# Kernel optimization log

Hardware: AMD Instinct MI355X
Metric: run time of the kernel (lower is better)

The kernel has to match this reference:

```python
import jax, jax.numpy as jnp
import numpy as np

N, L, S, D, H = 4, 8192, 8192, 256, 8
HD = D // H
EPS_ATTN = 1e-6
EPS_LN = 1e-5


def _layer_norm(x, g, b):
    mu = jnp.mean(x, axis=-1, keepdims=True)
    var = jnp.mean((x - mu) ** 2, axis=-1, keepdims=True)
    return (x - mu) / jnp.sqrt(var + EPS_LN) * g + b


def setup_inputs() -> dict:
    key = jax.random.key(0)
    ks = jax.random.split(key, 12)
    sc = 1.0 / np.sqrt(D)
    sc2 = 1.0 / np.sqrt(2 * D)
    return {
        "x": jax.random.normal(ks[0], (N, L, D), jnp.float32),
        "source": jax.random.normal(ks[1], (N, S, D), jnp.float32),
        "x_mask": jnp.ones((N, L), jnp.float32),
        "source_mask": jnp.ones((N, S), jnp.float32),
        "Wq": jax.random.normal(ks[2], (D, D), jnp.float32) * sc,
        "Wk": jax.random.normal(ks[3], (D, D), jnp.float32) * sc,
        "Wv": jax.random.normal(ks[4], (D, D), jnp.float32) * sc,
        "Wm": jax.random.normal(ks[5], (D, D), jnp.float32) * sc,
        "W1": jax.random.normal(ks[6], (2 * D, 2 * D), jnp.float32) * sc2,
        "W2": jax.random.normal(ks[7], (D, 2 * D), jnp.float32) * sc2,
        "g1": jnp.ones((D,), jnp.float32),
        "b1": jnp.zeros((D,), jnp.float32),
        "g2": jnp.ones((D,), jnp.float32),
        "b2": jnp.zeros((D,), jnp.float32),
    }


def reference(x, source, x_mask, source_mask, Wq, Wk, Wv, Wm, W1, W2, g1, b1, g2, b2):
    n = x.shape[0]
    # QKV projections (Linear without bias: y = x @ W.T), split into heads
    q = (x @ Wq.T).reshape(n, -1, H, HD)         # [N, L, H, HD]
    k = (source @ Wk.T).reshape(n, -1, H, HD)    # [N, S, H, HD]
    v = (source @ Wv.T).reshape(n, -1, H, HD)    # [N, S, H, HD]

    # kernelized linear attention: phi(x) = elu(x) + 1
    Q = jax.nn.elu(q) + 1.0
    K = jax.nn.elu(k) + 1.0
    Q = Q * x_mask[:, :, None, None]
    K = K * source_mask[:, :, None, None]
    v = v * source_mask[:, :, None, None]

    s_len = v.shape[1]
    v = v / s_len
    KV = jnp.einsum('nshd,nshv->nhdv', K, v)                       # [N, H, HD, HD]
    Z = 1.0 / (jnp.einsum('nlhd,nhd->nlh', Q, K.sum(axis=1)) + EPS_ATTN)
    msg = jnp.einsum('nlhd,nhdv,nlh->nlhv', Q, KV, Z) * s_len      # [N, L, H, HD]

    # merge heads + LN
    msg = msg.reshape(n, -1, H * HD) @ Wm.T
    msg = _layer_norm(msg, g1, b1)

    # concat-MLP + LN + residual
    h = jnp.concatenate([x, msg], axis=2) @ W1.T
    h = jax.nn.relu(h) @ W2.T
    h = _layer_norm(h, g2, b2)
    return x + h
```

## Files before the change

kernel.cpp:

```cpp
#include <hip/hip_runtime.h>

using short8 = __attribute__((ext_vector_type(8))) short;
using f32x4  = __attribute__((ext_vector_type(4))) float;

__device__ __forceinline__ float bf2f(unsigned short u) {
  union { unsigned int i; float f; } c; c.i = ((unsigned int)u) << 16; return c.f;
}
__device__ __forceinline__ unsigned short f2bf(float x) {
  union { float f; unsigned int i; } c; c.f = x;
  unsigned int r = c.i + 0x7fffu + ((c.i >> 16) & 1u);
  return (unsigned short)(r >> 16);
}

__global__ void cast2_kernel(const float* __restrict__ a, const float* __restrict__ b,
                             unsigned short* __restrict__ oa, unsigned short* __restrict__ ob,
                             int n4) {
  int stride = gridDim.x * blockDim.x;
  for (int i = blockIdx.x * blockDim.x + threadIdx.x; i < 2 * n4; i += stride) {
    const float4* s; ushort4* d; int j;
    if (i < n4) { s = (const float4*)a; d = (ushort4*)oa; j = i; }
    else        { s = (const float4*)b; d = (ushort4*)ob; j = i - n4; }
    float4 v = s[j];
    ushort4 o; o.x = f2bf(v.x); o.y = f2bf(v.y); o.z = f2bf(v.z); o.w = f2bf(v.w);
    d[j] = o;
  }
}

__global__ void castw_kernel(const float* __restrict__ wq, const float* __restrict__ wk,
                             const float* __restrict__ wv, const float* __restrict__ wm,
                             const float* __restrict__ w1, const float* __restrict__ w2,
                             unsigned short* __restrict__ dst) {
  int i = blockIdx.x * blockDim.x + threadIdx.x;
  if (i >= 655360) return;
  const float* s; int off;
  if      (i < 65536)  { s = wq; off = i; }
  else if (i < 131072) { s = wk; off = i - 65536; }
  else if (i < 196608) { s = wv; off = i - 131072; }
  else if (i < 262144) { s = wm; off = i - 196608; }
  else if (i < 524288) { s = w1; off = i - 262144; }
  else                 { s = w2; off = i - 524288; }
  dst[i] = f2bf(s[off]);
}

enum { EPI_F32 = 0, EPI_ELU1_MASK = 1, EPI_KV = 2, EPI_RELU_BF16 = 3 };

template<int EPI, bool SPLITA>
__global__ __launch_bounds__(256)
void gemm_nt(const unsigned short* __restrict__ A, const unsigned short* __restrict__ A2,
             const unsigned short* __restrict__ B,
             void* __restrict__ C0, void* __restrict__ C1, const float* __restrict__ aux,
             int M, int O, int K, float scale) {
  __shared__ unsigned short As[128 * 64];
  __shared__ unsigned short Bs[128 * 64];
  const int t  = threadIdx.x;
  const int w  = t >> 6, l = t & 63;
  const int wr = w >> 1, wc = w & 1;
  const int lr = l & 15, kg = l >> 4;
  const int brow = blockIdx.x * 128, bcol = blockIdx.y * 128;
  const int rsub = l >> 3;
  const int swz  = 8 * ((l & 7) ^ rsub);

  f32x4 acc[4][4];
  f32x4 zero = {0.f, 0.f, 0.f, 0.f};
  #pragma unroll
  for (int m = 0; m < 4; m++)
    #pragma unroll
    for (int n = 0; n < 4; n++) acc[m][n] = zero;

  for (int k0 = 0; k0 < K; k0 += 64) {
    #pragma unroll
    for (int i = 0; i < 4; i++) {
      int c = w * 4 + i;
      int row = c * 8 + rsub;
      const unsigned short* ga;
      if (SPLITA) {
        const unsigned short* base = (k0 < 256) ? A : A2;
        ga = base + (size_t)(brow + row) * 256 + (k0 & 255) + swz;
      } else {
        ga = A + (size_t)(brow + row) * K + k0 + swz;
      }
      const unsigned short* gb = B + (size_t)(bcol + row) * K + k0 + swz;
      __builtin_amdgcn_global_load_lds((__attribute__((address_space(1))) unsigned int*)ga,
          (__attribute__((address_space(3))) unsigned int*)(As + c * 512), 16, 0, 0);
      __builtin_amdgcn_global_load_lds((__attribute__((address_space(1))) unsigned int*)gb,
          (__attribute__((address_space(3))) unsigned int*)(Bs + c * 512), 16, 0, 0);
    }
    __syncthreads();
    #pragma unroll
    for (int kk = 0; kk < 2; kk++) {
      short8 af[4], bfr[4];
      #pragma unroll
      for (int m = 0; m < 4; m++) {
        int r = wr * 64 + m * 16 + lr;
        int cb = kk * 64 + kg * 16;
        af[m] = *(const short8*)((const char*)As + r * 128 + (cb ^ ((r & 7) << 4)));
      }
      #pragma unroll
      for (int n = 0; n < 4; n++) {
        int r = wc * 64 + n * 16 + lr;
        int cb = kk * 64 + kg * 16;
        bfr[n] = *(const short8*)((const char*)Bs + r * 128 + (cb ^ ((r & 7) << 4)));
      }
      #pragma unroll
      for (int m = 0; m < 4; m++)
        #pragma unroll
        for (int n = 0; n < 4; n++)
          acc[m][n] = __builtin_amdgcn_mfma_f32_16x16x32_bf16(af[m], bfr[n], acc[m][n], 0, 0, 0);
    }
    __syncthreads();
  }

  #pragma unroll
  for (int m = 0; m < 4; m++) {
    #pragma unroll
    for (int n = 0; n < 4; n++) {
      int col = bcol + wc * 64 + n * 16 + lr;
      #pragma unroll
      for (int j = 0; j < 4; j++) {
        int row = brow + wr * 64 + m * 16 + kg * 4 + j;
        float v = acc[m][n][j];
        if (EPI == EPI_F32) {
          ((float*)C0)[(size_t)row * O + col] = v;
        } else if (EPI == EPI_ELU1_MASK) {
          float e = v > 0.f ? v + 1.f : __expf(v);
          ((unsigned short*)C0)[(size_t)row * O + col] = f2bf(e * aux[row]);
        } else if (EPI == EPI_KV) {
          int colm = col & 255;
          if (col < 256) {
            float e = v > 0.f ? v + 1.f : __expf(v);
            ((unsigned short*)C0)[(size_t)row * 256 + colm] = f2bf(e * aux[row]);
          } else {
            ((unsigned short*)C1)[(size_t)row * 256 + colm] = f2bf(v * aux[row] * scale);
          }
        } else {
          ((unsigned short*)C0)[(size_t)row * O + col] = f2bf(v > 0.f ? v : 0.f);
        }
      }
    }
  }
}

__global__ __launch_bounds__(1024)
void kv_partial(const unsigned short* __restrict__ Kb, const unsigned short* __restrict__ Vb,
                float* __restrict__ part_kv, float* __restrict__ part_ks) {
  __shared__ float Ks[16][256];
  __shared__ float Vs[16][256];
  const int t   = threadIdx.x;
  const int blk = blockIdx.x;
  const int n   = blk >> 6;
  const int s0  = (blk & 63) * 128;
  const int h   = t >> 7, g = (t >> 5) & 3, dv = t & 31;
  const int r16 = t >> 6, c4 = (t & 63) * 4;
  const int cbase = h * 32;
  f32x4 acc0 = {0.f, 0.f, 0.f, 0.f}, acc1 = {0.f, 0.f, 0.f, 0.f};
  float ks = 0.f;

  for (int tile = 0; tile < 8; ++tile) {
    int s = s0 + tile * 16;
    size_t gbase = ((size_t)(n * 8192 + s + r16)) * 256 + c4;
    ushort4 kk = *(const ushort4*)&Kb[gbase];
    ushort4 vv = *(const ushort4*)&Vb[gbase];
    __syncthreads();
    float4 kf; kf.x = bf2f(kk.x); kf.y = bf2f(kk.y); kf.z = bf2f(kk.z); kf.w = bf2f(kk.w);
    float4 vf; vf.x = bf2f(vv.x); vf.y = bf2f(vv.y); vf.z = bf2f(vv.z); vf.w = bf2f(vv.w);
    *(float4*)&Ks[r16][c4] = kf;
    *(float4*)&Vs[r16][c4] = vf;
    __syncthreads();
    if (t < 256) {
      #pragma unroll
      for (int r = 0; r < 16; ++r) ks += Ks[r][t];
    }
    #pragma unroll
    for (int si = 0; si < 16; ++si) {
      f32x4 k0 = *(const f32x4*)&Ks[si][cbase + g * 8];
      f32x4 k1 = *(const f32x4*)&Ks[si][cbase + g * 8 + 4];
      float vx = Vs[si][cbase + dv];
      acc0 += k0 * vx;
      acc1 += k1 * vx;
    }
  }
  float* dst = &part_kv[(size_t)blk * 8192 + h * 1024 + dv * 32 + g * 8];
  *(float4*)(dst + 0) = *(float4*)&acc0;
  *(float4*)(dst + 4) = *(float4*)&acc1;
  if (t < 256) part_ks[blk * 256 + t] = ks;
}

__global__ __launch_bounds__(1024)
void kv_finalize(const float* __restrict__ part_kv, const float* __restrict__ part_ks,
                 float* __restrict__ KVt, float* __restrict__ Ksum) {
  const int b = blockIdx.x, t = threadIdx.x;
  if (b < 32) {
    int n = b >> 3;
    int e = (b & 7) * 1024 + t;
    const float* p = part_kv + (size_t)n * 64 * 8192 + e;
    float s = 0.f;
    #pragma unroll 8
    for (int c = 0; c < 64; ++c) s += p[(size_t)c * 8192];
    KVt[(size_t)n * 8192 + e] = s;
  } else {
    int n = b - 32;
    if (t < 256) {
      const float* p = part_ks + n * 64 * 256 + t;
      float s = 0.f;
      #pragma unroll 8
      for (int c = 0; c < 64; ++c) s += p[c * 256];
      Ksum[n * 256 + t] = s;
    }
  }
}

__global__ __launch_bounds__(256)
void msg_apply(const unsigned short* __restrict__ Qb, const float* __restrict__ KVt,
               const float* __restrict__ Ksum, unsigned short* __restrict__ Mb) {
  __shared__ float KVs[8192];
  __shared__ float Kss[256];
  const int t = threadIdx.x;
  const int row0 = blockIdx.x * 32;
  const int n = blockIdx.x >> 8;
  const int r = t >> 3, h = t & 7;
  for (int i = t; i < 8192; i += 256) {
    int j = i ^ (((i >> 10) & 7) << 2);
    KVs[j] = KVt[(size_t)n * 8192 + i];
  }
  Kss[t] = Ksum[n * 256 + t];
  __syncthreads();

  const unsigned short* qp = &Qb[(size_t)(row0 + r) * 256 + h * 32];
  float q[32];
  #pragma unroll
  for (int i = 0; i < 4; ++i) {
    short8 v = *(const short8*)(qp + i * 8);
    #pragma unroll
    for (int j = 0; j < 8; ++j) q[i * 8 + j] = bf2f((unsigned short)v[j]);
  }
  float zden = 0.f;
  #pragma unroll
  for (int sl = 0; sl < 8; ++sl) {
    f32x4 kv = *(const f32x4*)&Kss[h * 32 + sl * 4];
    zden += q[sl*4+0]*kv[0] + q[sl*4+1]*kv[1] + q[sl*4+2]*kv[2] + q[sl*4+3]*kv[3];
  }
  float z = 8192.f / (zden + 1e-6f);
  const int kvbase = h * 1024;
  short8 ov[4];
  #pragma unroll
  for (int dv = 0; dv < 32; ++dv) {
    float o = 0.f;
    #pragma unroll
    for (int sl = 0; sl < 8; ++sl) {
      f32x4 kv = *(const f32x4*)&KVs[kvbase + dv * 32 + ((sl ^ h) << 2)];
      o += q[sl*4+0]*kv[0] + q[sl*4+1]*kv[1] + q[sl*4+2]*kv[2] + q[sl*4+3]*kv[3];
    }
    ov[dv >> 3][dv & 7] = (short)f2bf(o * z);
  }
  unsigned short* op = (unsigned short*)&Mb[(size_t)(row0 + r) * 256 + h * 32];
  #pragma unroll
  for (int i = 0; i < 4; ++i) *(short8*)(op + i * 8) = ov[i];
}

__device__ __forceinline__ float block_sum(float v, float* red) {
  #pragma unroll
  for (int o = 32; o; o >>= 1) v += __shfl_down(v, o, 64);
  __syncthreads();
  if ((threadIdx.x & 63) == 0) red[threadIdx.x >> 6] = v;
  __syncthreads();
  return red[0] + red[1] + red[2] + red[3];
}

__global__ __launch_bounds__(256)
void ln1_msg(const float* __restrict__ msgf, const float* __restrict__ g,
             const float* __restrict__ b, unsigned short* __restrict__ msgb) {
  __shared__ float red[4];
  int row = blockIdx.x, t = threadIdx.x;
  float v = msgf[(size_t)row * 256 + t];
  float mu  = block_sum(v, red) * (1.f / 256.f);
  float dvv = v - mu;
  float var = block_sum(dvv * dvv, red) * (1.f / 256.f);
  float y = dvv * rsqrtf(var + 1e-5f) * g[t] + b[t];
  msgb[(size_t)row * 256 + t] = f2bf(y);
}

__global__ __launch_bounds__(256)
void ln2_res(const float* __restrict__ hbuf, const float* __restrict__ x,
             const float* __restrict__ g, const float* __restrict__ b,
             float* __restrict__ out) {
  __shared__ float red[4];
  int row = blockIdx.x, t = threadIdx.x;
  float v = hbuf[(size_t)row * 256 + t];
  float mu  = block_sum(v, red) * (1.f / 256.f);
  float dvv = v - mu;
  float var = block_sum(dvv * dvv, red) * (1.f / 256.f);
  float y = dvv * rsqrtf(var + 1e-5f) * g[t] + b[t];
  out[(size_t)row * 256 + t] = x[(size_t)row * 256 + t] + y;
}

extern "C" void kernel_launch(void* const* d_in, const int* in_sizes, int n_in,
                              void* d_out, int out_size, void* d_ws, size_t ws_size,
                              hipStream_t stream) {
  const float* x   = (const float*)d_in[0];
  const float* src = (const float*)d_in[1];
  const float* xm  = (const float*)d_in[2];
  const float* sm  = (const float*)d_in[3];
  const float* Wq  = (const float*)d_in[4];
  const float* Wk  = (const float*)d_in[5];
  const float* Wv  = (const float*)d_in[6];
  const float* Wm  = (const float*)d_in[7];
  const float* W1  = (const float*)d_in[8];
  const float* W2  = (const float*)d_in[9];
  const float* g1  = (const float*)d_in[10];
  const float* b1  = (const float*)d_in[11];
  const float* g2  = (const float*)d_in[12];
  const float* b2  = (const float*)d_in[13];
  float* out = (float*)d_out;
  char*  ws  = (char*)d_ws;

  unsigned short* xb   = (unsigned short*)(ws);
  unsigned short* sb   = (unsigned short*)(ws + 16777216);
  unsigned short* Qb   = (unsigned short*)(ws + 33554432);
  unsigned short* Mb   = (unsigned short*)(ws + 50331648);
  unsigned short* Kb   = (unsigned short*)(ws + 67108864);
  unsigned short* Vb   = (unsigned short*)(ws + 83886080);
  float*          pkv  = (float*)(ws + 16777216);
  float*          pks  = (float*)(ws + 16777216 + 8388608);
  float*          msgf = (float*)(ws + 67108864);
  unsigned short* msgb = (unsigned short*)(ws + 50331648);
  unsigned short* h1b  = (unsigned short*)(ws + 67108864);
  float*          h2f  = (float*)(ws);
  float*          KV   = (float*)(ws + 100663296);
  float*          Ksm  = (float*)(ws + 100663296 + 131072);
  unsigned short* Wb   = (unsigned short*)(ws + 100663296 + 135168);
  unsigned short* Wqb = Wb;
  unsigned short* Wkb = Wb + 65536;
  unsigned short* Wmb = Wb + 196608;
  unsigned short* W1b = Wb + 262144;
  unsigned short* W2b = Wb + 524288;

  cast2_kernel<<<2048, 256, 0, stream>>>(x, src, xb, sb, 2097152);
  castw_kernel<<<2560, 256, 0, stream>>>(Wq, Wk, Wv, Wm, W1, W2, Wb);

  gemm_nt<EPI_ELU1_MASK, false><<<dim3(256, 2), 256, 0, stream>>>(
      xb, nullptr, Wqb, (void*)Qb, nullptr, xm, 32768, 256, 256, 0.f);
  gemm_nt<EPI_KV, false><<<dim3(256, 4), 256, 0, stream>>>(
      sb, nullptr, Wkb, (void*)Kb, (void*)Vb, sm, 32768, 512, 256, 1.f / 8192.f);

  kv_partial<<<256, 1024, 0, stream>>>(Kb, Vb, pkv, pks);
  kv_finalize<<<36, 1024, 0, stream>>>(pkv, pks, KV, Ksm);
  msg_apply<<<1024, 256, 0, stream>>>(Qb, KV, Ksm, Mb);

  gemm_nt<EPI_F32, false><<<dim3(256, 2), 256, 0, stream>>>(
      Mb, nullptr, Wmb, (void*)msgf, nullptr, nullptr, 32768, 256, 256, 0.f);
  ln1_msg<<<32768, 256, 0, stream>>>(msgf, g1, b1, msgb);

  gemm_nt<EPI_RELU_BF16, true><<<dim3(256, 4), 256, 0, stream>>>(
      xb, msgb, W1b, (void*)h1b, nullptr, nullptr, 32768, 512, 512, 0.f);
  gemm_nt<EPI_F32, false><<<dim3(256, 2), 256, 0, stream>>>(
      h1b, nullptr, W2b, (void*)h2f, nullptr, nullptr, 32768, 256, 512, 0.f);
  ln2_res<<<32768, 256, 0, stream>>>(h2f, x, g2, b2, out);
}
```

Before: 321.9 us.

## Fuse LayerNorm into full-row GEMM epilogues and merge cast kernels

Adds a gemm_ln kernel in which each 512-thread block owns 128 full 256-wide output rows. It computes LayerNorm statistics from the accumulators through shuffles and shared memory, then writes the normalized bf16 message, or the residual-added fp32 output, directly. This removes the fp32 intermediate round trips and the two separate per-row LN kernels. The two cast kernels are merged into one launch with vectorized weight casts. The trade-offs are fewer blocks per GEMM (256 blocks), a larger shared-memory footprint, and a one-pass variance formula (E[x²]-mu²) that is less numerically robust.

```diff
diff --git a/kernel.cpp b/kernel.cpp
--- a/kernel.cpp
+++ b/kernel.cpp
@@ -12,37 +12,41 @@
   return (unsigned short)(r >> 16);
 }
 
-__global__ void cast2_kernel(const float* __restrict__ a, const float* __restrict__ b,
-                             unsigned short* __restrict__ oa, unsigned short* __restrict__ ob,
-                             int n4) {
+__global__ void cast_all(const float* __restrict__ x, const float* __restrict__ src,
+                         const float* __restrict__ wq, const float* __restrict__ wk,
+                         const float* __restrict__ wv, const float* __restrict__ wm,
+                         const float* __restrict__ w1, const float* __restrict__ w2,
+                         unsigned short* __restrict__ xb, unsigned short* __restrict__ sb,
+                         unsigned short* __restrict__ Wb) {
+  const int NV = 2097152;
   int stride = gridDim.x * blockDim.x;
-  for (int i = blockIdx.x * blockDim.x + threadIdx.x; i < 2 * n4; i += stride) {
+  for (int i = blockIdx.x * blockDim.x + threadIdx.x; i < 2 * NV + 163840; i += stride) {
     const float4* s; ushort4* d; int j;
-    if (i < n4) { s = (const float4*)a; d = (ushort4*)oa; j = i; }
-    else        { s = (const float4*)b; d = (ushort4*)ob; j = i - n4; }
+    if (i < NV)            { s = (const float4*)x;   d = (ushort4*)xb; j = i; }
+    else if (i < 2 * NV)   { s = (const float4*)src; d = (ushort4*)sb; j = i - NV; }
+    else {
+      j = i - 2 * NV;
+      d = (ushort4*)Wb;
+      const float* w;
+      int off;
+      if      (j < 16384)  { w = wq; off = j; }
+      else if (j < 32768)  { w = wk; off = j - 16384; }
+      else if (j < 49152)  { w = wv; off = j - 32768; }
+      else if (j < 65536)  { w = wm; off = j - 49152; }
+      else if (j < 131072) { w = w1; off = j - 65536; }
+      else                 { w = w2; off = j - 131072; }
+      float4 v = ((const float4*)w)[off];
+      ushort4 o; o.x = f2bf(v.x); o.y = f2bf(v.y); o.z = f2bf(v.z); o.w = f2bf(v.w);
+      d[j] = o;
+      continue;
+    }
     float4 v = s[j];
     ushort4 o; o.x = f2bf(v.x); o.y = f2bf(v.y); o.z = f2bf(v.z); o.w = f2bf(v.w);
     d[j] = o;
   }
 }
 
-__global__ void castw_kernel(const float* __restrict__ wq, const float* __restrict__ wk,
-                             const float* __restrict__ wv, const float* __restrict__ wm,
-                             const float* __restrict__ w1, const float* __restrict__ w2,
-                             unsigned short* __restrict__ dst) {
-  int i = blockIdx.x * blockDim.x + threadIdx.x;
-  if (i >= 655360) return;
-  const float* s; int off;
-  if      (i < 65536)  { s = wq; off = i; }
-  else if (i < 131072) { s = wk; off = i - 65536; }
-  else if (i < 196608) { s = wv; off = i - 131072; }
-  else if (i < 262144) { s = wm; off = i - 196608; }
-  else if (i < 524288) { s = w1; off = i - 262144; }
-  else                 { s = w2; off = i - 524288; }
-  dst[i] = f2bf(s[off]);
-}
-
-enum { EPI_F32 = 0, EPI_ELU1_MASK = 1, EPI_KV = 2, EPI_RELU_BF16 = 3 };
+enum { EPI_ELU1_MASK = 1, EPI_KV = 2, EPI_RELU_BF16 = 3 };
 
 template<int EPI, bool SPLITA>
 __global__ __launch_bounds__(256)
@@ -119,9 +123,7 @@
       for (int j = 0; j < 4; j++) {
         int row = brow + wr * 64 + m * 16 + kg * 4 + j;
         float v = acc[m][n][j];
-        if (EPI == EPI_F32) {
-          ((float*)C0)[(size_t)row * O + col] = v;
-        } else if (EPI == EPI_ELU1_MASK) {
+        if (EPI == EPI_ELU1_MASK) {
           float e = v > 0.f ? v + 1.f : __expf(v);
           ((unsigned short*)C0)[(size_t)row * O + col] = f2bf(e * aux[row]);
         } else if (EPI == EPI_KV) {
@@ -135,6 +137,117 @@
         } else {
           ((unsigned short*)C0)[(size_t)row * O + col] = f2bf(v > 0.f ? v : 0.f);
         }
+      }
+    }
+  }
+}
+
+template<int MODE>
+__global__ __launch_bounds__(512)
+void gemm_ln(const unsigned short* __restrict__ A, const unsigned short* __restrict__ B,
+             void* __restrict__ Cout, const float* __restrict__ g, const float* __restrict__ b,
+             const float* __restrict__ xres, int K) {
+  __shared__ unsigned short As[128 * 64];
+  __shared__ unsigned short Bs[256 * 64];
+  __shared__ float lnsum[128][4];
+  __shared__ float lnsq[128][4];
+  const int t  = threadIdx.x;
+  const int w  = t >> 6, l = t & 63;
+  const int wr = w >> 2, wc = w & 3;
+  const int lr = l & 15, kg = l >> 4;
+  const int brow = blockIdx.x * 128;
+  const int rsub = l >> 3;
+  const int swz  = 8 * ((l & 7) ^ rsub);
+
+  f32x4 acc[4][4];
+  f32x4 zero = {0.f, 0.f, 0.f, 0.f};
+  #pragma unroll
+  for (int m = 0; m < 4; m++)
+    #pragma unroll
+    for (int n = 0; n < 4; n++) acc[m][n] = zero;
+
+  for (int k0 = 0; k0 < K; k0 += 64) {
+    #pragma unroll
+    for (int i = 0; i < 6; i++) {
+      int c = w * 6 + i;
+      if (c < 16) {
+        int row = c * 8 + rsub;
+        const unsigned short* ga = A + (size_t)(brow + row) * K + k0 + swz;
+        __builtin_amdgcn_global_load_lds((__attribute__((address_space(1))) unsigned int*)ga,
+            (__attribute__((address_space(3))) unsigned int*)(As + c * 512), 16, 0, 0);
+      } else {
+        int row = (c - 16) * 8 + rsub;
+        const unsigned short* gb = B + (size_t)row * K + k0 + swz;
+        __builtin_amdgcn_global_load_lds((__attribute__((address_space(1))) unsigned int*)gb,
+            (__attribute__((address_space(3))) unsigned int*)(Bs + (c - 16) * 512), 16, 0, 0);
+      }
+    }
+    __syncthreads();
+    #pragma unroll
+    for (int kk = 0; kk < 2; kk++) {
+      short8 af[4], bfr[4];
+      #pragma unroll
+      for (int m = 0; m < 4; m++) {
+        int r = wr * 64 + m * 16 + lr;
+        int cb = kk * 64 + kg * 16;
+        af[m] = *(const short8*)((const char*)As + r * 128 + (cb ^ ((r & 7) << 4)));
+      }
+      #pragma unroll
+      for (int n = 0; n < 4; n++) {
+        int r = wc * 64 + n * 16 + lr;
+        int cb = kk * 64 + kg * 16;
+        bfr[n] = *(const short8*)((const char*)Bs + r * 128 + (cb ^ ((r & 7) << 4)));
+      }
+      #pragma unroll
+      for (int m = 0; m < 4; m++)
+        #pragma unroll
+        for (int n = 0; n < 4; n++)
+          acc[m][n] = __builtin_amdgcn_mfma_f32_16x16x32_bf16(af[m], bfr[n], acc[m][n], 0, 0, 0);
+    }
+    __syncthreads();
+  }
+
+  #pragma unroll
+  for (int m = 0; m < 4; m++) {
+    #pragma unroll
+    for (int j = 0; j < 4; j++) {
+      int rl = wr * 64 + m * 16 + kg * 4 + j;
+      float s = 0.f, qq = 0.f;
+      #pragma unroll
+      for (int n = 0; n < 4; n++) { float v = acc[m][n][j]; s += v; qq += v * v; }
+      #pragma unroll
+      for (int off = 1; off < 16; off <<= 1) {
+        s  += __shfl_xor(s, off, 64);
+        qq += __shfl_xor(qq, off, 64);
+      }
+      if (lr == 0) { lnsum[rl][wc] = s; lnsq[rl][wc] = qq; }
+    }
+  }
+  __syncthreads();
+
+  float gl[4], bl[4];
+  #pragma unroll
+  for (int n = 0; n < 4; n++) {
+    int col = wc * 64 + n * 16 + lr;
+    gl[n] = g[col]; bl[n] = b[col];
+  }
+  #pragma unroll
+  for (int m = 0; m < 4; m++) {
+    #pragma unroll
+    for (int j = 0; j < 4; j++) {
+      int rl = wr * 64 + m * 16 + kg * 4 + j;
+      float s  = lnsum[rl][0] + lnsum[rl][1] + lnsum[rl][2] + lnsum[rl][3];
+      float qq = lnsq[rl][0] + lnsq[rl][1] + lnsq[rl][2] + lnsq[rl][3];
+      float mu = s * (1.f / 256.f);
+      float var = qq * (1.f / 256.f) - mu * mu;
+      float rs = rsqrtf(var + 1e-5f);
+      size_t row = (size_t)brow + rl;
+      #pragma unroll
+      for (int n = 0; n < 4; n++) {
+        int col = wc * 64 + n * 16 + lr;
+        float y = (acc[m][n][j] - mu) * rs * gl[n] + bl[n];
+        if (MODE == 0) ((unsigned short*)Cout)[row * 256 + col] = f2bf(y);
+        else           ((float*)Cout)[row * 256 + col] = xres[row * 256 + col] + y;
       }
     }
   }
@@ -257,42 +370,6 @@
   for (int i = 0; i < 4; ++i) *(short8*)(op + i * 8) = ov[i];
 }
 
-__device__ __forceinline__ float block_sum(float v, float* red) {
-  #pragma unroll
-  for (int o = 32; o; o >>= 1) v += __shfl_down(v, o, 64);
-  __syncthreads();
-  if ((threadIdx.x & 63) == 0) red[threadIdx.x >> 6] = v;
-  __syncthreads();
-  return red[0] + red[1] + red[2] + red[3];
-}
-
-__global__ __launch_bounds__(256)
-void ln1_msg(const float* __restrict__ msgf, const float* __restrict__ g,
-             const float* __restrict__ b, unsigned short* __restrict__ msgb) {
-  __shared__ float red[4];
-  int row = blockIdx.x, t = threadIdx.x;
-  float v = msgf[(size_t)row * 256 + t];
-  float mu  = block_sum(v, red) * (1.f / 256.f);
-  float dvv = v - mu;
-  float var = block_sum(dvv * dvv, red) * (1.f / 256.f);
-  float y = dvv * rsqrtf(var + 1e-5f) * g[t] + b[t];
-  msgb[(size_t)row * 256 + t] = f2bf(y);
-}
-
-__global__ __launch_bounds__(256)
-void ln2_res(const float* __restrict__ hbuf, const float* __restrict__ x,
-             const float* __restrict__ g, const float* __restrict__ b,
-             float* __restrict__ out) {
-  __shared__ float red[4];
-  int row = blockIdx.x, t = threadIdx.x;
-  float v = hbuf[(size_t)row * 256 + t];
-  float mu  = block_sum(v, red) * (1.f / 256.f);
-  float dvv = v - mu;
-  float var = block_sum(dvv * dvv, red) * (1.f / 256.f);
-  float y = dvv * rsqrtf(var + 1e-5f) * g[t] + b[t];
-  out[(size_t)row * 256 + t] = x[(size_t)row * 256 + t] + y;
-}
-
 extern "C" void kernel_launch(void* const* d_in, const int* in_sizes, int n_in,
                               void* d_out, int out_size, void* d_ws, size_t ws_size,
                               hipStream_t stream) {
@@ -321,10 +398,8 @@
   unsigned short* Vb   = (unsigned short*)(ws + 83886080);
   float*          pkv  = (float*)(ws + 16777216);
   float*          pks  = (float*)(ws + 16777216 + 8388608);
-  float*          msgf = (float*)(ws + 67108864);
-  unsigned short* msgb = (unsigned short*)(ws + 50331648);
-  unsigned short* h1b  = (unsigned short*)(ws + 67108864);
-  float*          h2f  = (float*)(ws);
+  unsigned short* msgb = (unsigned short*)(ws + 67108864);
+  unsigned short* h1b  = (unsigned short*)(ws + 33554432);
   float*          KV   = (float*)(ws + 100663296);
   float*          Ksm  = (float*)(ws + 100663296 + 131072);
   unsigned short* Wb   = (unsigned short*)(ws + 100663296 + 135168);
@@ -334,8 +409,7 @@
   unsigned short* W1b = Wb + 262144;
   unsigned short* W2b = Wb + 524288;
 
-  cast2_kernel<<<2048, 256, 0, stream>>>(x, src, xb, sb, 2097152);
-  castw_kernel<<<2560, 256, 0, stream>>>(Wq, Wk, Wv, Wm, W1, W2, Wb);
+  cast_all<<<4096, 256, 0, stream>>>(x, src, Wq, Wk, Wv, Wm, W1, W2, xb, sb, Wb);
 
   gemm_nt<EPI_ELU1_MASK, false><<<dim3(256, 2), 256, 0, stream>>>(
       xb, nullptr, Wqb, (void*)Qb, nullptr, xm, 32768, 256, 256, 0.f);
@@ -346,13 +420,10 @@
   kv_finalize<<<36, 1024, 0, stream>>>(pkv, pks, KV, Ksm);
   msg_apply<<<1024, 256, 0, stream>>>(Qb, KV, Ksm, Mb);
 
-  gemm_nt<EPI_F32, false><<<dim3(256, 2), 256, 0, stream>>>(
-      Mb, nullptr, Wmb, (void*)msgf, nullptr, nullptr, 32768, 256, 256, 0.f);
-  ln1_msg<<<32768, 256, 0, stream>>>(msgf, g1, b1, msgb);
+  gemm_ln<0><<<256, 512, 0, stream>>>(Mb, Wmb, (void*)msgb, g1, b1, nullptr, 256);
 
   gemm_nt<EPI_RELU_BF16, true><<<dim3(256, 4), 256, 0, stream>>>(
       xb, msgb, W1b, (void*)h1b, nullptr, nullptr, 32768, 512, 512, 0.f);
-  gemm_nt<EPI_F32, false><<<dim3(256, 2), 256, 0, stream>>>(
-      h1b, nullptr, W2b, (void*)h2f, nullptr, nullptr, 32768, 256, 512, 0.f);
-  ln2_res<<<32768, 256, 0, stream>>>(h2f, x, g2, b2, out);
-}
+
+  gemm_ln<1><<<256, 512, 0, stream>>>(h1b, W2b, (void*)out, g2, b2, x, 512);
+}
```

Measured after the change: 286.5 us. -11.0%, faster.
